# Performance work log

Measured on AMD Instinct MI355X. Metric: run time of the kernel, lower is better.

Reference implementation:

```python
import jax, jax.numpy as jnp
import numpy as np

RADIUS = 0.4
NSAMPLE = 32
B, N, NPOINT, C = 4, 16384, 4096, 64


def _ball_query(xyz, new_xyz, radius, nsample):
    """PointNet++ ball query: first `nsample` point indices (in original order)
    within `radius` of each query; pad with the first found index (0 if none).
    xyz: (B,N,3)  new_xyz: (B,M,3)  ->  idx: (B,M,nsample) int32."""
    n = xyz.shape[1]
    # squared distances (B, M, N) via ||a||^2 + ||b||^2 - 2 a.b
    qq = jnp.sum(new_xyz * new_xyz, axis=-1)[:, :, None]
    pp = jnp.sum(xyz * xyz, axis=-1)[:, None, :]
    d2 = qq + pp - 2.0 * jnp.einsum('bmd,bnd->bmn', new_xyz, xyz)
    ar = jnp.arange(n, dtype=jnp.int32)
    # key = point index if inside ball else sentinel n; smallest keys = earliest hits
    key = jnp.where(d2 < radius * radius, ar, n)
    neg_small, _ = jax.lax.top_k(-key, nsample)   # nsample smallest keys
    sel = -neg_small                               # (B, M, nsample)
    valid = sel < n
    first = jnp.where(valid[..., :1], sel[..., :1], 0)
    return jnp.where(valid, sel, first).astype(jnp.int32)


def setup_inputs() -> dict:
    key = jax.random.key(0)
    k1, k2, k3 = jax.random.split(key, 3)
    xyz = jax.random.normal(k1, (B, N, 3), dtype=jnp.float32)
    new_xyz = jax.random.normal(k2, (B, NPOINT, 3), dtype=jnp.float32)
    features = jax.random.normal(k3, (B, C, N), dtype=jnp.float32)
    return {"xyz": xyz, "new_xyz": new_xyz, "features": features}


def reference(xyz, new_xyz, features):
    idx = _ball_query(xyz, new_xyz, RADIUS, NSAMPLE)            # (B, M, S)
    # gather xyz -> (B, M, S, 3) -> (B, 3, M, S), center on queries
    grouped_xyz = jax.vmap(lambda p, i: p[i])(xyz, idx)
    grouped_xyz = jnp.transpose(grouped_xyz, (0, 3, 1, 2))
    grouped_xyz = grouped_xyz - jnp.transpose(new_xyz, (0, 2, 1))[..., None]
    # gather features -> (B, C, M, S)
    grouped_feat = jax.vmap(lambda f, i: f[:, i])(features, idx)
    # use_xyz=True: concat centered coords with features on channel dim
    return jnp.concatenate([grouped_xyz, grouped_feat], axis=1)  # (B, 3+C, M, S)
```

## Files before the change

kernel.cpp:

```cpp
#include <hip/hip_runtime.h>
#include <stdint.h>

#define B_ 4
#define N_ 16384
#define M_ 4096
#define C_ 64
#define S_ 32
#define R2_ 0.16f
#define GDIM 32
#define CELLS 32768
#define CSTRIDE 32772

static const size_t OFF_XYZ4  = 0;
static const size_t OFF_FT    = (size_t)B_ * N_ * 4 * sizeof(float);
static const size_t OFF_START = OFF_FT + (size_t)B_ * N_ * C_ * sizeof(float);
static const size_t OFF_CUR   = OFF_START + (size_t)B_ * CSTRIDE * sizeof(int);
static const size_t OFF_SPTS  = OFF_CUR + (size_t)B_ * CSTRIDE * sizeof(int);
static const size_t OFF_SSID  = OFF_SPTS + (size_t)B_ * N_ * 4 * sizeof(float);

__device__ __forceinline__ int cellof(float v) {
    int c = (int)floorf((v + 8.0f) * 2.0f);
    return c < 0 ? 0 : (c > GDIM - 1 ? GDIM - 1 : c);
}

__global__ __launch_bounds__(256) void pack_hist(const float* __restrict__ xyz,
                                                 float4* __restrict__ xyz4,
                                                 int* __restrict__ cur) {
    int i = blockIdx.x * 256 + threadIdx.x;
    int b = i >> 14;
    float x = xyz[3 * i + 0];
    float y = xyz[3 * i + 1];
    float z = xyz[3 * i + 2];
    float pp = __fadd_rn(__fadd_rn(__fmul_rn(x, x), __fmul_rn(y, y)), __fmul_rn(z, z));
    xyz4[i] = make_float4(x, y, z, pp);
    int cid = (cellof(z) << 10) | (cellof(y) << 5) | cellof(x);
    atomicAdd(&cur[b * CSTRIDE + cid], 1);
}

__global__ __launch_bounds__(1024) void scan_cells(int* __restrict__ cur,
                                                   int* __restrict__ start) {
    __shared__ int ls[16];
    int b = blockIdx.x, t = threadIdx.x;
    int lane = t & 63, w = t >> 6;
    int* cb = cur + b * CSTRIDE;
    int* sb = start + b * CSTRIDE;
    int base = t * 32;
    int loc[32]; int tot = 0;
    #pragma unroll
    for (int j = 0; j < 32; ++j) { loc[j] = cb[base + j]; tot += loc[j]; }
    int pre = tot;
    #pragma unroll
    for (int o = 1; o < 64; o <<= 1) { int u = __shfl_up(pre, o); if (lane >= o) pre += u; }
    if (lane == 63) ls[w] = pre;
    __syncthreads();
    if (t < 16) {
        int v = ls[t];
        int p16 = v;
        #pragma unroll
        for (int o = 1; o < 16; o <<= 1) { int u = __shfl_up(p16, o); if (t >= o) p16 += u; }
        ls[t] = p16 - v;
    }
    __syncthreads();
    int run = ls[w] + (pre - tot);
    #pragma unroll
    for (int j = 0; j < 32; ++j) { sb[base + j] = run; cb[base + j] = run; run += loc[j]; }
    if (t == 0) sb[CELLS] = N_;
}

__global__ __launch_bounds__(256) void scatter_pts(const float4* __restrict__ xyz4,
                                                   int* __restrict__ cur,
                                                   float4* __restrict__ spts,
                                                   int* __restrict__ ssid) {
    int i = blockIdx.x * 256 + threadIdx.x;
    int b = i >> 14, n = i & (N_ - 1);
    float4 P = xyz4[i];
    int cid = (cellof(P.z) << 10) | (cellof(P.y) << 5) | cellof(P.x);
    int pos = atomicAdd(&cur[b * CSTRIDE + cid], 1);
    spts[(size_t)b * N_ + pos] = P;
    ssid[b * N_ + pos] = n;
}

__global__ __launch_bounds__(256) void transpose_feat(const float* __restrict__ f,
                                                      float* __restrict__ ft) {
    __shared__ float tile[64][65];
    int b  = blockIdx.x >> 8;
    int n0 = (blockIdx.x & 255) << 6;
    int tid  = threadIdx.x;
    int lane = tid & 63;
    int grp  = tid >> 6;
    #pragma unroll
    for (int r = 0; r < 16; ++r) {
        int c = r * 4 + grp;
        tile[c][lane] = f[((size_t)b * C_ + c) * N_ + n0 + lane];
    }
    __syncthreads();
    #pragma unroll
    for (int r = 0; r < 16; ++r) {
        int nl = r * 4 + grp;
        ft[((size_t)b * N_ + n0 + nl) * C_ + lane] = tile[lane][nl];
    }
}

__global__ __launch_bounds__(256) void bq_group(const float4* __restrict__ spts,
                                                const int* __restrict__ ssid,
                                                const int* __restrict__ start,
                                                const float* __restrict__ newxyz,
                                                const float4* __restrict__ xyz4,
                                                const float* __restrict__ ft,
                                                float* __restrict__ out) {
    __shared__ unsigned int bmAll[4][512];
    __shared__ int bcAll[4];
    int tid = threadIdx.x, lane = tid & 63, w = tid >> 6;
    unsigned int* bm = bmAll[w];
    int gw = blockIdx.x * 4 + w;
    int b = gw >> 12;
    int m = gw & (M_ - 1);

    *(uint4*)&bm[lane * 8]     = make_uint4(0u, 0u, 0u, 0u);
    *(uint4*)&bm[lane * 8 + 4] = make_uint4(0u, 0u, 0u, 0u);
    if (lane == 0) bcAll[w] = 0;

    size_t qb = ((size_t)b * M_ + m) * 3;
    float qx = newxyz[qb + 0], qy = newxyz[qb + 1], qz = newxyz[qb + 2];
    float qq = __fadd_rn(__fadd_rn(__fmul_rn(qx, qx), __fmul_rn(qy, qy)), __fmul_rn(qz, qz));
    int cx = cellof(qx), cy = cellof(qy), cz = cellof(qz);
    const float4* sp  = spts + (size_t)b * N_;
    const int*    sid = ssid + b * N_;
    const int*    st  = start + b * CSTRIDE;
    int x0 = cx > 0 ? cx - 1 : 0;
    int x1 = cx < GDIM - 1 ? cx + 1 : GDIM - 1;

    int sv = 0, ev = 0;
    if (lane < 9) {
        int dzi = lane / 3, dyi = lane - dzi * 3;
        int nz = cz + dzi - 1, ny = cy + dyi - 1;
        if ((unsigned)nz < GDIM && (unsigned)ny < GDIM) {
            int rowb = (nz << 10) | (ny << 5);
            sv = st[rowb | x0];
            ev = st[(rowb | x1) + 1];
        }
    }
    __builtin_amdgcn_wave_barrier();

    #pragma unroll 1
    for (int j = 0; j < 9; ++j) {
        int s = __shfl(sv, j);
        int e = __shfl(ev, j);
        for (int i = s + lane; i < e; i += 64) {
            float4 P = sp[i];
            float dot = __fmaf_rn(qz, P.z, __fmaf_rn(qy, P.y, __fmul_rn(qx, P.x)));
            float d2  = __fsub_rn(__fadd_rn(qq, P.w), __fmul_rn(2.0f, dot));
            if (d2 < R2_) {
                int o = sid[i];
                atomicOr(&bm[o >> 5], 1u << (o & 31));
            }
        }
    }
    __builtin_amdgcn_wave_barrier();

    uint4 a = *(const uint4*)&bm[lane * 8];
    uint4 c = *(const uint4*)&bm[lane * 8 + 4];
    unsigned int wds[8] = {a.x, a.y, a.z, a.w, c.x, c.y, c.z, c.w};
    int tl = 0;
    #pragma unroll
    for (int j = 0; j < 8; ++j) tl += __popc(wds[j]);
    int pre = tl;
    #pragma unroll
    for (int o = 1; o < 64; o <<= 1) { int u = __shfl_up(pre, o); if (lane >= o) pre += u; }
    int cnt = __shfl(pre, 63);
    int r = pre - tl;
    int basei = lane << 8;
    __builtin_amdgcn_wave_barrier();
    int* sel = (int*)bm;
    #pragma unroll
    for (int wd = 0; wd < 8; ++wd) {
        if (r >= S_) break;
        unsigned int bits = wds[wd];
        while (bits && r < S_) {
            int bpos = __builtin_ctz(bits);
            bits &= bits - 1;
            int gidx = basei + (wd << 5) + bpos;
            if (r == 0) bcAll[w] = gidx;
            sel[r] = gidx;
            ++r;
        }
    }
    __builtin_amdgcn_wave_barrier();
    if (lane < S_ && lane >= cnt) sel[lane] = bcAll[w];
    __builtin_amdgcn_wave_barrier();

    int s    = lane & 31;
    int half = lane >> 5;
    int p    = sel[s];
    const float* fp = ft + (((size_t)b * N_ + p) << 6) + half * 32;
    float4 v[8];
    #pragma unroll
    for (int j = 0; j < 8; ++j) v[j] = *(const float4*)(fp + j * 4);

    const size_t cst = (size_t)M_ * S_;
    size_t ob = (((size_t)b * 67 + 3 + half * 32) * M_ + m) * S_ + s;
    #pragma unroll
    for (int j = 0; j < 8; ++j) {
        out[ob + (4 * j + 0) * cst] = v[j].x;
        out[ob + (4 * j + 1) * cst] = v[j].y;
        out[ob + (4 * j + 2) * cst] = v[j].z;
        out[ob + (4 * j + 3) * cst] = v[j].w;
    }
    if (half == 0) {
        float4 P = xyz4[(size_t)b * N_ + p];
        size_t xb = (((size_t)b * 67 + 0) * M_ + m) * S_ + s;
        out[xb + 0 * cst] = P.x - qx;
        out[xb + 1 * cst] = P.y - qy;
        out[xb + 2 * cst] = P.z - qz;
    }
}

extern "C" void kernel_launch(void* const* d_in, const int* in_sizes, int n_in,
                              void* d_out, int out_size, void* d_ws, size_t ws_size,
                              hipStream_t stream) {
    const float* xyz    = (const float*)d_in[0];
    const float* newxyz = (const float*)d_in[1];
    const float* feat   = (const float*)d_in[2];
    float* out = (float*)d_out;

    char* ws = (char*)d_ws;
    float4* xyz4  = (float4*)(ws + OFF_XYZ4);
    float*  ft    = (float*)(ws + OFF_FT);
    int*    startc= (int*)(ws + OFF_START);
    int*    curc  = (int*)(ws + OFF_CUR);
    float4* spts  = (float4*)(ws + OFF_SPTS);
    int*    ssid  = (int*)(ws + OFF_SSID);

    hipMemsetAsync(curc, 0, (size_t)B_ * CSTRIDE * sizeof(int), stream);
    pack_hist     <<<(B_ * N_) / 256, 256, 0, stream>>>(xyz, xyz4, curc);
    scan_cells    <<<B_, 1024, 0, stream>>>(curc, startc);
    scatter_pts   <<<(B_ * N_) / 256, 256, 0, stream>>>(xyz4, curc, spts, ssid);
    transpose_feat<<<B_ * (N_ / 64), 256, 0, stream>>>(feat, ft);
    bq_group      <<<(B_ * M_) / 4, 256, 0, stream>>>(spts, ssid, startc, newxyz,
                                                      xyz4, ft, out);
}
```

Measured before the change: 220.6 us.

## Fuse histogram with feature transpose, prune grid cells, use nontemporal stores

Merges the point-packing histogram kernel and the feature transpose into one launch, removing one kernel launch and letting the two independent jobs run together. Ball-query cell ranges are trimmed per z/y row, using the distance from the query to each row's box to drop x-cells that cannot lie inside the radius. The sorted-index load is hoisted ahead of the distance test, and output and input streams use nontemporal loads and stores to reduce cache pollution. The pruning depends on epsilon margins to keep exact results at cell boundaries, and the fused kernel now has divergent block roles.

```diff
diff --git a/kernel.cpp b/kernel.cpp
--- a/kernel.cpp
+++ b/kernel.cpp
@@ -23,18 +23,41 @@
     return c < 0 ? 0 : (c > GDIM - 1 ? GDIM - 1 : c);
 }
 
-__global__ __launch_bounds__(256) void pack_hist(const float* __restrict__ xyz,
-                                                 float4* __restrict__ xyz4,
-                                                 int* __restrict__ cur) {
-    int i = blockIdx.x * 256 + threadIdx.x;
-    int b = i >> 14;
-    float x = xyz[3 * i + 0];
-    float y = xyz[3 * i + 1];
-    float z = xyz[3 * i + 2];
-    float pp = __fadd_rn(__fadd_rn(__fmul_rn(x, x), __fmul_rn(y, y)), __fmul_rn(z, z));
-    xyz4[i] = make_float4(x, y, z, pp);
-    int cid = (cellof(z) << 10) | (cellof(y) << 5) | cellof(x);
-    atomicAdd(&cur[b * CSTRIDE + cid], 1);
+__global__ __launch_bounds__(256) void pack_hist_transpose(const float* __restrict__ xyz,
+                                                           float4* __restrict__ xyz4,
+                                                           int* __restrict__ cur,
+                                                           const float* __restrict__ f,
+                                                           float* __restrict__ ft) {
+    if (blockIdx.x < 256) {
+        int i = blockIdx.x * 256 + threadIdx.x;
+        int b = i >> 14;
+        float x = __builtin_nontemporal_load(&xyz[3 * i + 0]);
+        float y = __builtin_nontemporal_load(&xyz[3 * i + 1]);
+        float z = __builtin_nontemporal_load(&xyz[3 * i + 2]);
+        float pp = __fadd_rn(__fadd_rn(__fmul_rn(x, x), __fmul_rn(y, y)), __fmul_rn(z, z));
+        xyz4[i] = make_float4(x, y, z, pp);
+        int cid = (cellof(z) << 10) | (cellof(y) << 5) | cellof(x);
+        atomicAdd(&cur[b * CSTRIDE + cid], 1);
+    } else {
+        __shared__ float tile[64][65];
+        int blk = blockIdx.x - 256;
+        int b  = blk >> 8;
+        int n0 = (blk & 255) << 6;
+        int tid  = threadIdx.x;
+        int lane = tid & 63;
+        int grp  = tid >> 6;
+        #pragma unroll
+        for (int r = 0; r < 16; ++r) {
+            int c = r * 4 + grp;
+            tile[c][lane] = __builtin_nontemporal_load(&f[((size_t)b * C_ + c) * N_ + n0 + lane]);
+        }
+        __syncthreads();
+        #pragma unroll
+        for (int r = 0; r < 16; ++r) {
+            int nl = r * 4 + grp;
+            ft[((size_t)b * N_ + n0 + nl) * C_ + lane] = tile[lane][nl];
+        }
+    }
 }
 
 __global__ __launch_bounds__(1024) void scan_cells(int* __restrict__ cur,
@@ -78,27 +101,6 @@
     int pos = atomicAdd(&cur[b * CSTRIDE + cid], 1);
     spts[(size_t)b * N_ + pos] = P;
     ssid[b * N_ + pos] = n;
-}
-
-__global__ __launch_bounds__(256) void transpose_feat(const float* __restrict__ f,
-                                                      float* __restrict__ ft) {
-    __shared__ float tile[64][65];
-    int b  = blockIdx.x >> 8;
-    int n0 = (blockIdx.x & 255) << 6;
-    int tid  = threadIdx.x;
-    int lane = tid & 63;
-    int grp  = tid >> 6;
-    #pragma unroll
-    for (int r = 0; r < 16; ++r) {
-        int c = r * 4 + grp;
-        tile[c][lane] = f[((size_t)b * C_ + c) * N_ + n0 + lane];
-    }
-    __syncthreads();
-    #pragma unroll
-    for (int r = 0; r < 16; ++r) {
-        int nl = r * 4 + grp;
-        ft[((size_t)b * N_ + n0 + nl) * C_ + lane] = tile[lane][nl];
-    }
 }
 
 __global__ __launch_bounds__(256) void bq_group(const float4* __restrict__ spts,
@@ -135,9 +137,26 @@
         int dzi = lane / 3, dyi = lane - dzi * 3;
         int nz = cz + dzi - 1, ny = cy + dyi - 1;
         if ((unsigned)nz < GDIM && (unsigned)ny < GDIM) {
-            int rowb = (nz << 10) | (ny << 5);
-            sv = st[rowb | x0];
-            ev = st[(rowb | x1) + 1];
+            float zlo = (nz == 0)        ? -1e30f : -8.0f + 0.5f * nz;
+            float zhi = (nz == GDIM - 1) ?  1e30f : -8.0f + 0.5f * (nz + 1);
+            float ylo = (ny == 0)        ? -1e30f : -8.0f + 0.5f * ny;
+            float yhi = (ny == GDIM - 1) ?  1e30f : -8.0f + 0.5f * (ny + 1);
+            float dz = fmaxf(fmaxf(zlo - qz, qz - zhi), 0.0f);
+            float dy = fmaxf(fmaxf(ylo - qy, qy - yhi), 0.0f);
+            float rem = R2_ + 1e-3f - dz * dz - dy * dy;
+            if (rem > 0.0f) {
+                float rx = sqrtf(rem) + 1e-3f;
+                int xl = (int)floorf((qx - rx + 8.0f) * 2.0f);
+                int xh = (int)floorf((qx + rx + 8.0f) * 2.0f);
+                xl = xl < 0 ? 0 : xl;  xh = xh > GDIM - 1 ? GDIM - 1 : xh;
+                xl = xl > x0 ? xl : x0;
+                xh = xh < x1 ? xh : x1;
+                if (xl <= xh) {
+                    int rowb = (nz << 10) | (ny << 5);
+                    sv = st[rowb | xl];
+                    ev = st[(rowb | xh) + 1];
+                }
+            }
         }
     }
     __builtin_amdgcn_wave_barrier();
@@ -148,10 +167,10 @@
         int e = __shfl(ev, j);
         for (int i = s + lane; i < e; i += 64) {
             float4 P = sp[i];
+            int o = sid[i];
             float dot = __fmaf_rn(qz, P.z, __fmaf_rn(qy, P.y, __fmul_rn(qx, P.x)));
             float d2  = __fsub_rn(__fadd_rn(qq, P.w), __fmul_rn(2.0f, dot));
             if (d2 < R2_) {
-                int o = sid[i];
                 atomicOr(&bm[o >> 5], 1u << (o & 31));
             }
         }
@@ -201,17 +220,17 @@
     size_t ob = (((size_t)b * 67 + 3 + half * 32) * M_ + m) * S_ + s;
     #pragma unroll
     for (int j = 0; j < 8; ++j) {
-        out[ob + (4 * j + 0) * cst] = v[j].x;
-        out[ob + (4 * j + 1) * cst] = v[j].y;
-        out[ob + (4 * j + 2) * cst] = v[j].z;
-        out[ob + (4 * j + 3) * cst] = v[j].w;
+        __builtin_nontemporal_store(v[j].x, &out[ob + (4 * j + 0) * cst]);
+        __builtin_nontemporal_store(v[j].y, &out[ob + (4 * j + 1) * cst]);
+        __builtin_nontemporal_store(v[j].z, &out[ob + (4 * j + 2) * cst]);
+        __builtin_nontemporal_store(v[j].w, &out[ob + (4 * j + 3) * cst]);
     }
     if (half == 0) {
         float4 P = xyz4[(size_t)b * N_ + p];
         size_t xb = (((size_t)b * 67 + 0) * M_ + m) * S_ + s;
-        out[xb + 0 * cst] = P.x - qx;
-        out[xb + 1 * cst] = P.y - qy;
-        out[xb + 2 * cst] = P.z - qz;
+        __builtin_nontemporal_store(P.x - qx, &out[xb + 0 * cst]);
+        __builtin_nontemporal_store(P.y - qy, &out[xb + 1 * cst]);
+        __builtin_nontemporal_store(P.z - qz, &out[xb + 2 * cst]);
     }
 }
 
@@ -232,10 +251,9 @@
     int*    ssid  = (int*)(ws + OFF_SSID);
 
     hipMemsetAsync(curc, 0, (size_t)B_ * CSTRIDE * sizeof(int), stream);
-    pack_hist     <<<(B_ * N_) / 256, 256, 0, stream>>>(xyz, xyz4, curc);
+    pack_hist_transpose<<<256 + B_ * (N_ / 64), 256, 0, stream>>>(xyz, xyz4, curc, feat, ft);
     scan_cells    <<<B_, 1024, 0, stream>>>(curc, startc);
     scatter_pts   <<<(B_ * N_) / 256, 256, 0, stream>>>(xyz4, curc, spts, ssid);
-    transpose_feat<<<B_ * (N_ / 64), 256, 0, stream>>>(feat, ft);
     bq_group      <<<(B_ * M_) / 4, 256, 0, stream>>>(spts, ssid, startc, newxyz,
                                                       xyz4, ft, out);
 }
```

After: 218.1 us. About the same (-1.1%).
